# Kernel optimization log

Hardware: AMD Instinct MI355X
Metric: run time of the kernel (lower is better)

The kernel has to match this reference:

```python
import jax, jax.numpy as jnp
import numpy as np

B, C, D_IN, D_H, D_QK = 64, 512, 1024, 1024, 512
EPS = 1e-5


def setup_inputs() -> dict:
    key = jax.random.key(0)
    ks = jax.random.split(key, 24)
    din2 = D_IN + D_H  # concat([x, h]) feature dim
    s_qk = 1.0 / np.sqrt(din2)
    inp = {
        "x": jax.random.normal(ks[0], (B, C, D_IN), jnp.float32),
        "h": jax.random.normal(ks[1], (B, C, D_H), jnp.float32),
    }
    i = 2
    for g in ("r", "z", "n"):
        inp[f"Wq_{g}"] = jax.random.normal(ks[i], (din2, D_QK), jnp.float32) * s_qk; i += 1
        inp[f"bq_{g}"] = jnp.zeros((D_QK,), jnp.float32)
        inp[f"Wk_{g}"] = jax.random.normal(ks[i], (din2, D_QK), jnp.float32) * s_qk; i += 1
        inp[f"bk_{g}"] = jnp.zeros((D_QK,), jnp.float32)
        inp[f"Wv_{g}"] = jax.random.normal(ks[i], (din2, D_H), jnp.float32) * s_qk; i += 1
        inp[f"bv_{g}"] = jnp.zeros((D_H,), jnp.float32)
    inp["gamma"] = jnp.ones((D_H,), jnp.float32)
    inp["beta"] = jnp.zeros((D_H,), jnp.float32)
    return inp


def _self_attention(xin, Wq, bq, Wk, bk, Wv, bv):
    # xin: (B, C, 2D) ; attention over channel axis C
    Q = xin @ Wq + bq            # (B, C, d_qk)
    K = xin @ Wk + bk            # (B, C, d_qk)
    V = xin @ Wv + bv            # (B, C, d_h)
    scale = 1.0 / jnp.sqrt(jnp.asarray(Q.shape[-1], jnp.float32))
    scores = jnp.einsum("bcd,bed->bce", Q, K) * scale   # (B, C, C)
    attn = jax.nn.softmax(scores, axis=-1)
    return jnp.einsum("bce,bed->bcd", attn, V)          # (B, C, d_h)


def reference(x, h,
              Wq_r, bq_r, Wk_r, bk_r, Wv_r, bv_r,
              Wq_z, bq_z, Wk_z, bk_z, Wv_z, bv_z,
              Wq_n, bq_n, Wk_n, bk_n, Wv_n, bv_n,
              gamma, beta):
    xh = jnp.concatenate([x, h], axis=2)
    r = _self_attention(xh, Wq_r, bq_r, Wk_r, bk_r, Wv_r, bv_r)
    z = _self_attention(xh, Wq_z, bq_z, Wk_z, bk_z, Wv_z, bv_z)
    reset = jax.nn.sigmoid(r)
    update = jax.nn.sigmoid(z)
    xhr = jnp.concatenate([x, h * reset], axis=2)
    n = _self_attention(xhr, Wq_n, bq_n, Wk_n, bk_n, Wv_n, bv_n)
    new_state = (1.0 - update) * h + update * jnp.tanh(n)
    # LayerNorm over last dim
    mu = jnp.mean(new_state, axis=-1, keepdims=True)
    var = jnp.var(new_state, axis=-1, keepdims=True)
    return (new_state - mu) * jax.lax.rsqrt(var + EPS) * gamma + beta
```

## Files before the change

### kernel.cpp

```cpp
#include <hip/hip_runtime.h>
#include <math.h>

typedef __attribute__((ext_vector_type(8))) short short8;
typedef __attribute__((ext_vector_type(4))) float f32x4;

#define EPI_QKV   0
#define EPI_PEXP  1
#define EPI_R     2
#define EPI_Z     3
#define EPI_N     4

__device__ __forceinline__ unsigned short f2bf(float f) {
    unsigned int u = __float_as_uint(f);
    u += 0x7fffu + ((u >> 16) & 1u);
    return (unsigned short)(u >> 16);
}
__device__ __forceinline__ float bf2f(unsigned short s) {
    return __uint_as_float(((unsigned int)s) << 16);
}

struct alignas(8) us4 { unsigned short a, b, c, d; };

#define GLD_LDS16(gp, lp) \
    __builtin_amdgcn_global_load_lds((const __attribute__((address_space(1))) unsigned int*)(gp), \
                                     (__attribute__((address_space(3))) unsigned int*)(lp), 16, 0, 0)

#define BAR   do { asm volatile("" ::: "memory"); __builtin_amdgcn_s_barrier(); \
                   asm volatile("" ::: "memory"); } while (0)
#define VMC4  asm volatile("s_waitcnt vmcnt(4)" ::: "memory")
#define VMC0  asm volatile("s_waitcnt vmcnt(0)" ::: "memory")

template<int EPI, int SWZ>
__global__ void __launch_bounds__(512, 2)
gemm256(const unsigned short* __restrict__ A, long long sAb, int lda,
        const unsigned short* __restrict__ Bt, long long sBb, int ldb,
        const float* __restrict__ bias,
        void* __restrict__ C, long long sCb, int ldc,
        int K, float scale,
        const float* __restrict__ hptr,
        const unsigned short* __restrict__ updptr,
        float* __restrict__ psum,
        unsigned short* __restrict__ vt)
{
    extern __shared__ char smem[];

    const int z = blockIdx.z;
    A  += (size_t)z * (size_t)sAb;
    Bt += (size_t)z * (size_t)sBb;

    int bx, by;
    if (SWZ) {
        const int bid = blockIdx.y * 8 + blockIdx.x;
        const int xcd = bid & 7, i = bid >> 3;
        bx = i & 7;
        by = (xcd << 4) | (i >> 3);
    } else {
        bx = blockIdx.x; by = blockIdx.y;
    }
    const int m0 = by * 256;
    const int n0 = bx * 256;

    const int tid = threadIdx.x;
    const int w  = tid >> 6;
    const int l  = tid & 63;
    const int wr = w >> 2;
    const int wc = w & 3;
    const int lr = l & 15;
    const int lg = l >> 4;
    const int rs = (lr & 7) << 4;

    const int srw = l >> 3;
    const int scb = ((l & 7) << 4) ^ (srw << 4);

    const long long ldab = (long long)lda * 2;
    const long long ldbb = (long long)ldb * 2;

    f32x4 acc[2][4][4] = {};
    short8 a[4][2], b[4][2];

#define STAGE1(gbase, ldbytes, grow0, ldsoff) { \
    const char* g_ = (const char*)(gbase) + \
        (size_t)((grow0) + w*8 + srw) * (ldbytes) + scb; \
    GLD_LDS16(g_, smem + (ldsoff) + (w << 10)); }

#define AOFF(buf) ((buf)*65536)
#define BOFF(buf) ((buf)*65536 + 32768)

#define LDA8(MH, buf) { \
    const char* Ab_ = smem + AOFF(buf); \
    _Pragma("unroll") \
    for (int mf = 0; mf < 4; ++mf) { \
        const int row_ = wr*128 + (MH)*64 + mf*16 + lr; \
        _Pragma("unroll") \
        for (int kk = 0; kk < 2; ++kk) \
            a[mf][kk] = *(const short8*)(Ab_ + row_*128 + ((kk*64 + lg*16) ^ rs)); } }

#define LDB4(BH, buf) { \
    const char* Bb_ = smem + BOFF(buf); \
    _Pragma("unroll") \
    for (int nf = 0; nf < 2; ++nf) { \
        const int row_ = wc*64 + (BH)*32 + nf*16 + lr; \
        _Pragma("unroll") \
        for (int kk = 0; kk < 2; ++kk) \
            b[(BH)*2+nf][kk] = *(const short8*)(Bb_ + row_*128 + ((kk*64 + lg*16) ^ rs)); } }

#define MMA16(MH, BH) { \
    __builtin_amdgcn_s_setprio(1); \
    _Pragma("unroll") \
    for (int kk = 0; kk < 2; ++kk) \
    _Pragma("unroll") \
    for (int mf = 0; mf < 4; ++mf) \
    _Pragma("unroll") \
    for (int nf = 0; nf < 2; ++nf) \
        acc[MH][mf][(BH)*2+nf] = __builtin_amdgcn_mfma_f32_16x16x32_bf16( \
            a[mf][kk], b[(BH)*2+nf][kk], acc[MH][mf][(BH)*2+nf], 0, 0, 0); \
    __builtin_amdgcn_s_setprio(0); }

    {
        STAGE1(A,        ldab, m0 + 0,   AOFF(0) + 0);
        STAGE1(A,        ldab, m0 + 128, AOFF(0) + 16384);
        STAGE1(A,        ldab, m0 + 64,  AOFF(0) + 8192);
        STAGE1(A,        ldab, m0 + 192, AOFF(0) + 24576);
        STAGE1(Bt,       ldbb, n0 + 0,   BOFF(0) + 0);
        STAGE1(Bt,       ldbb, n0 + 128, BOFF(0) + 16384);
        STAGE1(Bt,       ldbb, n0 + 64,  BOFF(0) + 8192);
        STAGE1(Bt,       ldbb, n0 + 192, BOFF(0) + 24576);
        STAGE1(A + 64,   ldab, m0 + 0,   AOFF(1) + 0);
        STAGE1(A + 64,   ldab, m0 + 128, AOFF(1) + 16384);
        STAGE1(A + 64,   ldab, m0 + 64,  AOFF(1) + 8192);
        STAGE1(A + 64,   ldab, m0 + 192, AOFF(1) + 24576);
        VMC4;
        BAR;
    }

    const int NT = K >> 6;
    for (int t = 0; t < NT; ++t) {
        const int p = t & 1, q = p ^ 1;
        const unsigned short* An = A  + (size_t)(t + 2) * 64;
        const unsigned short* Bn = Bt + (size_t)(t + 1) * 64;
        const bool sB = (t + 1 < NT), sA = (t + 2 < NT);

        LDA8(0, p); LDB4(0, p);
        if (sB) { STAGE1(Bn, ldbb, n0 + 0,   BOFF(q) + 0);
                  STAGE1(Bn, ldbb, n0 + 128, BOFF(q) + 16384); }
        BAR;
        MMA16(0, 0);
        LDB4(1, p);
        if (sB) { STAGE1(Bn, ldbb, n0 + 64,  BOFF(q) + 8192);
                  STAGE1(Bn, ldbb, n0 + 192, BOFF(q) + 24576); }
        BAR;
        MMA16(0, 1);
        LDA8(1, p);
        if (sA) { STAGE1(An, ldab, m0 + 0,   AOFF(p) + 0);
                  STAGE1(An, ldab, m0 + 128, AOFF(p) + 16384); }
        BAR;
        MMA16(1, 1);
        BAR;
        if (sA) { STAGE1(An, ldab, m0 + 64,  AOFF(p) + 8192);
                  STAGE1(An, ldab, m0 + 192, AOFF(p) + 24576);
                  VMC4; }
        else if (sB) { VMC0; }
        BAR;
        MMA16(1, 0);
    }

    const int Mb = gridDim.y << 8;
    const size_t zc = (size_t)z * (size_t)sCb;

    if (EPI == EPI_PEXP) {
        float psl[2][4][4];
        #pragma unroll
        for (int mh = 0; mh < 2; ++mh)
            #pragma unroll
            for (int mf = 0; mf < 4; ++mf)
                #pragma unroll
                for (int r = 0; r < 4; ++r) psl[mh][mf][r] = 0.0f;

        #pragma unroll
        for (int mh = 0; mh < 2; ++mh)
        #pragma unroll
        for (int mf = 0; mf < 4; ++mf)
        #pragma unroll
        for (int nf = 0; nf < 4; ++nf) {
            const int col = n0 + wc * 64 + nf * 16 + lr;
            #pragma unroll
            for (int r = 0; r < 4; ++r) {
                const int row = m0 + wr * 128 + mh * 64 + mf * 16 + lg * 4 + r;
                const float e = __expf(acc[mh][mf][nf][r] * scale);
                ((unsigned short*)C)[zc + (size_t)row * ldc + col] = f2bf(e);
                psl[mh][mf][r] += e;
            }
        }
        #pragma unroll
        for (int d = 1; d < 16; d <<= 1)
            #pragma unroll
            for (int mh = 0; mh < 2; ++mh)
                #pragma unroll
                for (int mf = 0; mf < 4; ++mf)
                    #pragma unroll
                    for (int r = 0; r < 4; ++r)
                        psl[mh][mf][r] += __shfl_xor(psl[mh][mf][r], d);
        __syncthreads();
        float* red = (float*)smem;
        if (lr == 0) {
            #pragma unroll
            for (int mh = 0; mh < 2; ++mh)
                #pragma unroll
                for (int mf = 0; mf < 4; ++mf)
                    #pragma unroll
                    for (int r = 0; r < 4; ++r)
                        red[wc * 256 + wr * 128 + mh * 64 + mf * 16 + lg * 4 + r]
                            = psl[mh][mf][r];
        }
        __syncthreads();
        if (tid < 256) {
            const float sres = red[tid] + red[256 + tid] + red[512 + tid] + red[768 + tid];
            psum[(size_t)bx * 32768 + (size_t)z * 512 + m0 + tid] = sres;
        }
        return;
    }

    float invs[2][4][4];
    if (EPI == EPI_R || EPI == EPI_Z || EPI == EPI_N) {
        #pragma unroll
        for (int mh = 0; mh < 2; ++mh)
            #pragma unroll
            for (int mf = 0; mf < 4; ++mf)
                #pragma unroll
                for (int r = 0; r < 4; ++r) {
                    const int row = m0 + wr * 128 + mh * 64 + mf * 16 + lg * 4 + r;
                    const size_t gr = (size_t)z * 512 + row;
                    invs[mh][mf][r] = 1.0f / (psum[gr] + psum[32768 + gr]);
                }
    }

    #pragma unroll
    for (int mh = 0; mh < 2; ++mh) {
        #pragma unroll
        for (int mf = 0; mf < 4; ++mf) {
            #pragma unroll
            for (int nf = 0; nf < 4; ++nf) {
                const int col = n0 + wc * 64 + nf * 16 + lr;
                const float bval = (EPI == EPI_QKV) ? bias[col] : 0.0f;
                if (EPI == EPI_QKV && bx >= 4) {
                    const int row0 = m0 + wr * 128 + mh * 64 + mf * 16 + lg * 4;
                    us4 o = { f2bf(acc[mh][mf][nf][0] + bval),
                              f2bf(acc[mh][mf][nf][1] + bval),
                              f2bf(acc[mh][mf][nf][2] + bval),
                              f2bf(acc[mh][mf][nf][3] + bval) };
                    *(us4*)(vt + (size_t)(row0 >> 9) * 524288 +
                            (size_t)(col - 1024) * 512 + (row0 & 511)) = o;
                } else {
                    #pragma unroll
                    for (int r = 0; r < 4; ++r) {
                        const int row = m0 + wr * 128 + mh * 64 + mf * 16 + lg * 4 + r;
                        float v = acc[mh][mf][nf][r] + bval;
                        if (EPI == EPI_QKV) {
                            ((unsigned short*)C)[(size_t)row * ldc + col] = f2bf(v);
                        } else if (EPI == EPI_R) {
                            v *= invs[mh][mf][r];
                            const size_t flat = (size_t)z * Mb + row;
                            const float hh = hptr[flat * 1024 + col];
                            const float sg = 1.0f / (1.0f + __expf(-v));
                            ((unsigned short*)C)[flat * 2048 + 1024 + col] = f2bf(hh * sg);
                        } else if (EPI == EPI_Z) {
                            v *= invs[mh][mf][r];
                            const size_t flat = (size_t)z * Mb + row;
                            const float sg = 1.0f / (1.0f + __expf(-v));
                            ((unsigned short*)C)[flat * 1024 + col] = f2bf(sg);
                        } else {
                            v *= invs[mh][mf][r];
                            const size_t flat = (size_t)z * Mb + row;
                            const float u  = bf2f(updptr[flat * 1024 + col]);
                            const float hh = hptr[flat * 1024 + col];
                            ((float*)C)[flat * 1024 + col] = (1.0f - u) * hh + u * tanhf(v);
                        }
                    }
                }
            }
        }
    }
#undef STAGE1
#undef AOFF
#undef BOFF
#undef LDA8
#undef LDB4
#undef MMA16
}


__global__ void __launch_bounds__(256)
prep_xh(const float* __restrict__ x, const float* __restrict__ h, unsigned short* __restrict__ xh)
{
    const size_t t = (size_t)blockIdx.x * 256 + threadIdx.x;
    const size_t f = t * 4;
    const size_t row = f >> 10, col = f & 1023;
    const float4 vx = *(const float4*)(x + f);
    const float4 vh = *(const float4*)(h + f);
    us4 ox = { f2bf(vx.x), f2bf(vx.y), f2bf(vx.z), f2bf(vx.w) };
    us4 oh = { f2bf(vh.x), f2bf(vh.y), f2bf(vh.z), f2bf(vh.w) };
    *(us4*)(xh + row * 2048 + col)        = ox;
    *(us4*)(xh + row * 2048 + 1024 + col) = oh;
}

__global__ void __launch_bounds__(256)
transpose_w(const float* __restrict__ W, unsigned short* __restrict__ WT, int N)
{
    __shared__ float t[32][33];
    const int k0 = blockIdx.y * 32, n0 = blockIdx.x * 32;
    const int tx = threadIdx.x & 31, ty = threadIdx.x >> 5;
    #pragma unroll
    for (int i = 0; i < 4; ++i)
        t[ty + i * 8][tx] = W[(size_t)(k0 + ty + i * 8) * N + n0 + tx];
    __syncthreads();
    #pragma unroll
    for (int i = 0; i < 4; ++i)
        WT[(size_t)(n0 + ty + i * 8) * 2048 + k0 + tx] = f2bf(t[tx][ty + i * 8]);
}

__global__ void __launch_bounds__(256)
layernorm1024(float* __restrict__ Y, const float* __restrict__ gamma, const float* __restrict__ beta)
{
    const int row = blockIdx.x * 4 + (threadIdx.x >> 6);
    const int l = threadIdx.x & 63;
    float* p = Y + (size_t)row * 1024;
    float4 v[4];
    float s = 0.0f, s2 = 0.0f;
    #pragma unroll
    for (int i = 0; i < 4; ++i) {
        v[i] = ((const float4*)p)[i * 64 + l];
        s  += v[i].x + v[i].y + v[i].z + v[i].w;
        s2 += v[i].x * v[i].x + v[i].y * v[i].y + v[i].z * v[i].z + v[i].w * v[i].w;
    }
    #pragma unroll
    for (int d = 32; d; d >>= 1) { s += __shfl_xor(s, d); s2 += __shfl_xor(s2, d); }
    const float mu = s * (1.0f / 1024.0f);
    const float var = s2 * (1.0f / 1024.0f) - mu * mu;
    const float inv = rsqrtf(var + 1e-5f);
    #pragma unroll
    for (int i = 0; i < 4; ++i) {
        const float4 gv = ((const float4*)gamma)[i * 64 + l];
        const float4 bv = ((const float4*)beta)[i * 64 + l];
        float4 o;
        o.x = (v[i].x - mu) * inv * gv.x + bv.x;
        o.y = (v[i].y - mu) * inv * gv.y + bv.y;
        o.z = (v[i].z - mu) * inv * gv.z + bv.z;
        o.w = (v[i].w - mu) * inv * gv.w + bv.w;
        ((float4*)p)[i * 64 + l] = o;
    }
}

__global__ void __launch_bounds__(256)
concat_bias(const float* __restrict__ a, const float* __restrict__ b,
            const float* __restrict__ c, float* __restrict__ o)
{
    const int i = blockIdx.x * 256 + threadIdx.x;
    o[i] = (i < 512) ? a[i] : (i < 1024) ? b[i - 512] : c[i - 1024];
}

extern "C" void kernel_launch(void* const* d_in, const int* in_sizes, int n_in,
                              void* d_out, int out_size, void* d_ws, size_t ws_size,
                              hipStream_t stream)
{
    (void)in_sizes; (void)n_in; (void)out_size; (void)ws_size;

    const float* x = (const float*)d_in[0];
    const float* h = (const float*)d_in[1];
    const float* Wf[9]; const float* bia[9];
    for (int g = 0; g < 3; ++g)
        for (int j = 0; j < 3; ++j) {
            Wf[g * 3 + j]  = (const float*)d_in[2 + g * 6 + j * 2];
            bia[g * 3 + j] = (const float*)d_in[2 + g * 6 + j * 2 + 1];
        }
    const float* gamma = (const float*)d_in[20];
    const float* beta  = (const float*)d_in[21];
    float* out = (float*)d_out;

    const int LDS_BYTES = 131072;
    hipFuncSetAttribute((const void*)gemm256<EPI_QKV, 1>,  hipFuncAttributeMaxDynamicSharedMemorySize, LDS_BYTES);
    hipFuncSetAttribute((const void*)gemm256<EPI_PEXP, 0>, hipFuncAttributeMaxDynamicSharedMemorySize, LDS_BYTES);
    hipFuncSetAttribute((const void*)gemm256<EPI_R, 0>,    hipFuncAttributeMaxDynamicSharedMemorySize, LDS_BYTES);
    hipFuncSetAttribute((const void*)gemm256<EPI_Z, 0>,    hipFuncAttributeMaxDynamicSharedMemorySize, LDS_BYTES);
    hipFuncSetAttribute((const void*)gemm256<EPI_N, 0>,    hipFuncAttributeMaxDynamicSharedMemorySize, LDS_BYTES);

    char* ws = (char*)d_ws;
    size_t off = 0;
    auto alloc = [&](size_t bytes) -> void* {
        void* p = ws + off; off += (bytes + 255) & ~(size_t)255; return p;
    };
    unsigned short* xh  = (unsigned short*)alloc((size_t)32768 * 2048 * 2);
    unsigned short* WT  = (unsigned short*)alloc((size_t)12582912 * 2);
    unsigned short* QK  = (unsigned short*)alloc((size_t)32768 * 1024 * 2);
    unsigned short* Vt  = (unsigned short*)alloc((size_t)32768 * 1024 * 2);
    unsigned short* Pb  = (unsigned short*)alloc((size_t)64 * 512 * 512 * 2);
    unsigned short* upd = (unsigned short*)alloc((size_t)32768 * 1024 * 2);
    float*          psb = (float*)alloc((size_t)2 * 32768 * 4);
    float*          bct = (float*)alloc((size_t)3 * 2048 * 4);

    size_t wtoff[9];
    {
        size_t o = 0;
        for (int g = 0; g < 3; ++g) {
            wtoff[g * 3 + 0] = o; o += (size_t)512 * 2048;
            wtoff[g * 3 + 1] = o; o += (size_t)512 * 2048;
            wtoff[g * 3 + 2] = o; o += (size_t)1024 * 2048;
        }
    }

    prep_xh<<<32768, 256, 0, stream>>>(x, h, xh);
    for (int i = 0; i < 9; ++i) {
        const int N = (i % 3 == 2) ? 1024 : 512;
        transpose_w<<<dim3(N / 32, 64, 1), 256, 0, stream>>>(Wf[i], WT + wtoff[i], N);
    }
    for (int g = 0; g < 3; ++g)
        concat_bias<<<8, 256, 0, stream>>>(bia[g * 3 + 0], bia[g * 3 + 1], bia[g * 3 + 2], bct + g * 2048);

    const float scscale = 0.044194173824159216f;

    auto gate = [&](int g, int epi) {
        const unsigned short* wT = WT + wtoff[g * 3 + 0];
        gemm256<EPI_QKV, 1><<<dim3(8, 128, 1), 512, LDS_BYTES, stream>>>(
            xh, 0, 2048, wT, 0, 2048, bct + g * 2048,
            QK, 0, 1024, 2048, 0.0f, nullptr, nullptr, nullptr, Vt);
        gemm256<EPI_PEXP, 0><<<dim3(2, 2, 64), 512, LDS_BYTES, stream>>>(
            QK, 524288, 1024, QK + 512, 524288, 1024, nullptr,
            Pb, 262144, 512, 512, scscale, nullptr, nullptr, psb, nullptr);
        if (epi == EPI_Z)
            gemm256<EPI_Z, 0><<<dim3(4, 2, 64), 512, LDS_BYTES, stream>>>(
                Pb, 262144, 512, Vt, 524288, 512, nullptr,
                upd, 0, 1024, 512, 0.0f, nullptr, nullptr, psb, nullptr);
        else if (epi == EPI_R)
            gemm256<EPI_R, 0><<<dim3(4, 2, 64), 512, LDS_BYTES, stream>>>(
                Pb, 262144, 512, Vt, 524288, 512, nullptr,
                xh, 0, 2048, 512, 0.0f, h, nullptr, psb, nullptr);
        else
            gemm256<EPI_N, 0><<<dim3(4, 2, 64), 512, LDS_BYTES, stream>>>(
                Pb, 262144, 512, Vt, 524288, 512, nullptr,
                out, 0, 1024, 512, 0.0f, h, upd, psb, nullptr);
    };

    gate(1, EPI_Z);
    gate(0, EPI_R);
    gate(2, EPI_N);
    layernorm1024<<<8192, 256, 0, stream>>>(out, gamma, beta);
}
```

Baseline: 1.295 ms.

## Restructure GEMM main loop with double-buffered fragment registers and finer prefetch

The 256x256 GEMM main loop is reordered so LDS fragment reads for the next MMA quarter are issued before the current MFMA block, using separate a0/a1/b0/b1 register sets. The B tile staging layout changes so each half of B (32-row groups per wave column) lands contiguously, and vmcnt waits are tuned to keep more global loads in flight. This aims to overlap LDS reads and global loads with MFMA work more tightly, at the cost of higher register pressure and a more fragile wait/barrier ordering.

```diff
diff --git a/kernel.cpp b/kernel.cpp
--- a/kernel.cpp
+++ b/kernel.cpp
@@ -27,7 +27,9 @@
 
 #define BAR   do { asm volatile("" ::: "memory"); __builtin_amdgcn_s_barrier(); \
                    asm volatile("" ::: "memory"); } while (0)
+#define VMC6  asm volatile("s_waitcnt vmcnt(6)" ::: "memory")
 #define VMC4  asm volatile("s_waitcnt vmcnt(4)" ::: "memory")
+#define VMC2  asm volatile("s_waitcnt vmcnt(2)" ::: "memory")
 #define VMC0  asm volatile("s_waitcnt vmcnt(0)" ::: "memory")
 
 template<int EPI, int SWZ>
@@ -71,40 +73,55 @@
 
     const int srw = l >> 3;
     const int scb = ((l & 7) << 4) ^ (srw << 4);
+    const int sbrow = ((w >> 2) << 6) + ((w & 3) << 3);
 
     const long long ldab = (long long)lda * 2;
     const long long ldbb = (long long)ldb * 2;
 
     f32x4 acc[2][4][4] = {};
-    short8 a[4][2], b[4][2];
+    short8 a0[4][2], a1[4][2], b0[2][2], b1[2][2];
 
 #define STAGE1(gbase, ldbytes, grow0, ldsoff) { \
     const char* g_ = (const char*)(gbase) + \
         (size_t)((grow0) + w*8 + srw) * (ldbytes) + scb; \
     GLD_LDS16(g_, smem + (ldsoff) + (w << 10)); }
 
+#define STAGE1B(gbase, grow0, ldsoff) { \
+    const char* g_ = (const char*)(gbase) + \
+        (size_t)((grow0) + sbrow + srw) * ldbb + scb; \
+    GLD_LDS16(g_, smem + (ldsoff) + (w << 10)); }
+
 #define AOFF(buf) ((buf)*65536)
 #define BOFF(buf) ((buf)*65536 + 32768)
 
-#define LDA8(MH, buf) { \
+#define SA0(buf, base) { STAGE1(base, ldab, m0 + 0,   AOFF(buf) + 0); \
+                         STAGE1(base, ldab, m0 + 128, AOFF(buf) + 16384); }
+#define SA1(buf, base) { STAGE1(base, ldab, m0 + 64,  AOFF(buf) + 8192); \
+                         STAGE1(base, ldab, m0 + 192, AOFF(buf) + 24576); }
+#define SB0(buf, base) { STAGE1B(base, n0 + 0,   BOFF(buf) + 0); \
+                         STAGE1B(base, n0 + 128, BOFF(buf) + 8192); }
+#define SB1(buf, base) { STAGE1B(base, n0 + 32,  BOFF(buf) + 16384); \
+                         STAGE1B(base, n0 + 160, BOFF(buf) + 24576); }
+
+#define LDA(dst, MH, buf) { \
     const char* Ab_ = smem + AOFF(buf); \
     _Pragma("unroll") \
     for (int mf = 0; mf < 4; ++mf) { \
         const int row_ = wr*128 + (MH)*64 + mf*16 + lr; \
         _Pragma("unroll") \
         for (int kk = 0; kk < 2; ++kk) \
-            a[mf][kk] = *(const short8*)(Ab_ + row_*128 + ((kk*64 + lg*16) ^ rs)); } }
-
-#define LDB4(BH, buf) { \
-    const char* Bb_ = smem + BOFF(buf); \
+            dst[mf][kk] = *(const short8*)(Ab_ + row_*128 + ((kk*64 + lg*16) ^ rs)); } }
+
+#define LDB(dst, BH, buf) { \
+    const char* Bb_ = smem + BOFF(buf) + (BH)*16384; \
     _Pragma("unroll") \
     for (int nf = 0; nf < 2; ++nf) { \
-        const int row_ = wc*64 + (BH)*32 + nf*16 + lr; \
+        const int row_ = wc*32 + nf*16 + lr; \
         _Pragma("unroll") \
         for (int kk = 0; kk < 2; ++kk) \
-            b[(BH)*2+nf][kk] = *(const short8*)(Bb_ + row_*128 + ((kk*64 + lg*16) ^ rs)); } }
-
-#define MMA16(MH, BH) { \
+            dst[nf][kk] = *(const short8*)(Bb_ + row_*128 + ((kk*64 + lg*16) ^ rs)); } }
+
+#define MMA(MH, BH, av, bv) { \
     __builtin_amdgcn_s_setprio(1); \
     _Pragma("unroll") \
     for (int kk = 0; kk < 2; ++kk) \
@@ -113,55 +130,43 @@
     _Pragma("unroll") \
     for (int nf = 0; nf < 2; ++nf) \
         acc[MH][mf][(BH)*2+nf] = __builtin_amdgcn_mfma_f32_16x16x32_bf16( \
-            a[mf][kk], b[(BH)*2+nf][kk], acc[MH][mf][(BH)*2+nf], 0, 0, 0); \
+            av[mf][kk], bv[nf][kk], acc[MH][mf][(BH)*2+nf], 0, 0, 0); \
     __builtin_amdgcn_s_setprio(0); }
 
-    {
-        STAGE1(A,        ldab, m0 + 0,   AOFF(0) + 0);
-        STAGE1(A,        ldab, m0 + 128, AOFF(0) + 16384);
-        STAGE1(A,        ldab, m0 + 64,  AOFF(0) + 8192);
-        STAGE1(A,        ldab, m0 + 192, AOFF(0) + 24576);
-        STAGE1(Bt,       ldbb, n0 + 0,   BOFF(0) + 0);
-        STAGE1(Bt,       ldbb, n0 + 128, BOFF(0) + 16384);
-        STAGE1(Bt,       ldbb, n0 + 64,  BOFF(0) + 8192);
-        STAGE1(Bt,       ldbb, n0 + 192, BOFF(0) + 24576);
-        STAGE1(A + 64,   ldab, m0 + 0,   AOFF(1) + 0);
-        STAGE1(A + 64,   ldab, m0 + 128, AOFF(1) + 16384);
-        STAGE1(A + 64,   ldab, m0 + 64,  AOFF(1) + 8192);
-        STAGE1(A + 64,   ldab, m0 + 192, AOFF(1) + 24576);
-        VMC4;
-        BAR;
-    }
+    SA0(0, A); SB0(0, Bt); SA1(0, A); SB1(0, Bt);
+    SA0(1, A + 64);
+    VMC6;
+    BAR;
+    LDA(a0, 0, 0);
+    LDB(b0, 0, 0);
 
     const int NT = K >> 6;
     for (int t = 0; t < NT; ++t) {
         const int p = t & 1, q = p ^ 1;
-        const unsigned short* An = A  + (size_t)(t + 2) * 64;
-        const unsigned short* Bn = Bt + (size_t)(t + 1) * 64;
-        const bool sB = (t + 1 < NT), sA = (t + 2 < NT);
-
-        LDA8(0, p); LDB4(0, p);
-        if (sB) { STAGE1(Bn, ldbb, n0 + 0,   BOFF(q) + 0);
-                  STAGE1(Bn, ldbb, n0 + 128, BOFF(q) + 16384); }
+        const bool s1 = (t + 1 < NT), s2 = (t + 2 < NT);
+        const unsigned short* Anx = A  + (size_t)(t + 1) * 64;
+        const unsigned short* Bnx = Bt + (size_t)(t + 1) * 64;
+        const unsigned short* Anx2 = A + (size_t)(t + 2) * 64;
+
+        if (t == NT - 1) { VMC0; } else { VMC2; }
         BAR;
-        MMA16(0, 0);
-        LDB4(1, p);
-        if (sB) { STAGE1(Bn, ldbb, n0 + 64,  BOFF(q) + 8192);
-                  STAGE1(Bn, ldbb, n0 + 192, BOFF(q) + 24576); }
+        LDB(b1, 1, p);
+        if (s1) { SB0(q, Bnx); }
+        MMA(0, 0, a0, b0);
         BAR;
-        MMA16(0, 1);
-        LDA8(1, p);
-        if (sA) { STAGE1(An, ldab, m0 + 0,   AOFF(p) + 0);
-                  STAGE1(An, ldab, m0 + 128, AOFF(p) + 16384); }
+        LDA(a1, 1, p);
+        if (s1) { SA1(q, Anx); }
+        MMA(0, 1, a0, b1);
+        VMC4;
         BAR;
-        MMA16(1, 1);
+        if (s1) { LDA(a0, 0, q); }
+        if (s1) { SB1(q, Bnx); }
+        MMA(1, 0, a1, b0);
+        VMC4;
         BAR;
-        if (sA) { STAGE1(An, ldab, m0 + 64,  AOFF(p) + 8192);
-                  STAGE1(An, ldab, m0 + 192, AOFF(p) + 24576);
-                  VMC4; }
-        else if (sB) { VMC0; }
-        BAR;
-        MMA16(1, 0);
+        if (s1) { LDB(b0, 0, q); }
+        if (s2) { SA0(p, Anx2); }
+        MMA(1, 1, a1, b1);
     }
 
     const int Mb = gridDim.y << 8;
@@ -281,11 +286,16 @@
         }
     }
 #undef STAGE1
+#undef STAGE1B
 #undef AOFF
 #undef BOFF
-#undef LDA8
-#undef LDB4
-#undef MMA16
+#undef SA0
+#undef SA1
+#undef SB0
+#undef SB1
+#undef LDA
+#undef LDB
+#undef MMA
 }
 
 
```

After: 1.323 ms. +2.1%, slower.

## Simplify GEMM main loop to plain double-buffered prefetch with one barrier

Applied to the files above, without the earlier changes.

Replaces the interleaved, staggered A/B LDS staging (A prefetched two tiles ahead, B one ahead, several barriers per K-step with partial vmcnt waits) with a simple scheme. The whole next A and B tile is prefetched into the other buffer at the start of each iteration, all four MMA quadrants run on the current buffer, and one full vmcnt(0) wait plus one barrier closes the step. This cuts per-iteration barrier count and scheduling complexity. In exchange it loses the finer-grained overlap and the deeper A prefetch, and the full drain wait at each step may expose memory latency.

```diff
diff --git a/kernel.cpp b/kernel.cpp
--- a/kernel.cpp
+++ b/kernel.cpp
@@ -27,7 +27,6 @@
 
 #define BAR   do { asm volatile("" ::: "memory"); __builtin_amdgcn_s_barrier(); \
                    asm volatile("" ::: "memory"); } while (0)
-#define VMC4  asm volatile("s_waitcnt vmcnt(4)" ::: "memory")
 #define VMC0  asm volatile("s_waitcnt vmcnt(0)" ::: "memory")
 
 template<int EPI, int SWZ>
@@ -86,6 +85,15 @@
 #define AOFF(buf) ((buf)*65536)
 #define BOFF(buf) ((buf)*65536 + 32768)
 
+#define SA(buf, base) { STAGE1(base, ldab, m0 + 0,   AOFF(buf) + 0); \
+                        STAGE1(base, ldab, m0 + 64,  AOFF(buf) + 8192); \
+                        STAGE1(base, ldab, m0 + 128, AOFF(buf) + 16384); \
+                        STAGE1(base, ldab, m0 + 192, AOFF(buf) + 24576); }
+#define SB(buf, base) { STAGE1(base, ldbb, n0 + 0,   BOFF(buf) + 0); \
+                        STAGE1(base, ldbb, n0 + 64,  BOFF(buf) + 8192); \
+                        STAGE1(base, ldbb, n0 + 128, BOFF(buf) + 16384); \
+                        STAGE1(base, ldbb, n0 + 192, BOFF(buf) + 24576); }
+
 #define LDA8(MH, buf) { \
     const char* Ab_ = smem + AOFF(buf); \
     _Pragma("unroll") \
@@ -116,52 +124,24 @@
             a[mf][kk], b[(BH)*2+nf][kk], acc[MH][mf][(BH)*2+nf], 0, 0, 0); \
     __builtin_amdgcn_s_setprio(0); }
 
-    {
-        STAGE1(A,        ldab, m0 + 0,   AOFF(0) + 0);
-        STAGE1(A,        ldab, m0 + 128, AOFF(0) + 16384);
-        STAGE1(A,        ldab, m0 + 64,  AOFF(0) + 8192);
-        STAGE1(A,        ldab, m0 + 192, AOFF(0) + 24576);
-        STAGE1(Bt,       ldbb, n0 + 0,   BOFF(0) + 0);
-        STAGE1(Bt,       ldbb, n0 + 128, BOFF(0) + 16384);
-        STAGE1(Bt,       ldbb, n0 + 64,  BOFF(0) + 8192);
-        STAGE1(Bt,       ldbb, n0 + 192, BOFF(0) + 24576);
-        STAGE1(A + 64,   ldab, m0 + 0,   AOFF(1) + 0);
-        STAGE1(A + 64,   ldab, m0 + 128, AOFF(1) + 16384);
-        STAGE1(A + 64,   ldab, m0 + 64,  AOFF(1) + 8192);
-        STAGE1(A + 64,   ldab, m0 + 192, AOFF(1) + 24576);
-        VMC4;
-        BAR;
-    }
+    SA(0, A); SB(0, Bt);
+    VMC0;
+    BAR;
 
     const int NT = K >> 6;
     for (int t = 0; t < NT; ++t) {
         const int p = t & 1, q = p ^ 1;
-        const unsigned short* An = A  + (size_t)(t + 2) * 64;
-        const unsigned short* Bn = Bt + (size_t)(t + 1) * 64;
-        const bool sB = (t + 1 < NT), sA = (t + 2 < NT);
-
-        LDA8(0, p); LDB4(0, p);
-        if (sB) { STAGE1(Bn, ldbb, n0 + 0,   BOFF(q) + 0);
-                  STAGE1(Bn, ldbb, n0 + 128, BOFF(q) + 16384); }
+        const bool s1 = (t + 1 < NT);
+        const unsigned short* Anx = A  + (size_t)(t + 1) * 64;
+        const unsigned short* Bnx = Bt + (size_t)(t + 1) * 64;
+
+        if (s1) { SA(q, Anx); SB(q, Bnx); }
+        LDA8(0, p); LDB4(0, p); LDB4(1, p);
+        MMA16(0, 0); MMA16(0, 1);
+        LDA8(1, p);
+        MMA16(1, 0); MMA16(1, 1);
+        VMC0;
         BAR;
-        MMA16(0, 0);
-        LDB4(1, p);
-        if (sB) { STAGE1(Bn, ldbb, n0 + 64,  BOFF(q) + 8192);
-                  STAGE1(Bn, ldbb, n0 + 192, BOFF(q) + 24576); }
-        BAR;
-        MMA16(0, 1);
-        LDA8(1, p);
-        if (sA) { STAGE1(An, ldab, m0 + 0,   AOFF(p) + 0);
-                  STAGE1(An, ldab, m0 + 128, AOFF(p) + 16384); }
-        BAR;
-        MMA16(1, 1);
-        BAR;
-        if (sA) { STAGE1(An, ldab, m0 + 64,  AOFF(p) + 8192);
-                  STAGE1(An, ldab, m0 + 192, AOFF(p) + 24576);
-                  VMC4; }
-        else if (sB) { VMC0; }
-        BAR;
-        MMA16(1, 0);
     }
 
     const int Mb = gridDim.y << 8;
@@ -283,6 +263,8 @@
 #undef STAGE1
 #undef AOFF
 #undef BOFF
+#undef SA
+#undef SB
 #undef LDA8
 #undef LDB4
 #undef MMA16
```

Measured after the change: 1.308 ms. Within noise of the previous version (+1.0%).
